# Kernel optimization log

Hardware: AMD Instinct MI355X
Metric: run time of the kernel (lower is better)

The kernel has to match this reference:

```python
import jax, jax.numpy as jnp
import numpy as np

N = 16384
M = 4096

def setup_inputs() -> dict:
    key = jax.random.key(0)
    kA, kB = jax.random.split(key)
    A = jax.random.normal(kA, (N,), dtype=jnp.float32)
    B = jax.random.normal(kB, (N, M), dtype=jnp.float32)
    return {"A": A, "B": B}

def reference(A, B):
    # C = diag(A) @ B == scale row i of B by A[i]
    return A[:, None] * B
```

## Files before the change

kernel.cpp:

```cpp
#include <hip/hip_runtime.h>


__global__ __launch_bounds__(256) void rowscale_f4_kernel(
    const float* __restrict__ A,
    const float4* __restrict__ B,
    float4* __restrict__ C,
    unsigned int nvec,
    unsigned int row_shift)
{
    unsigned int i = blockIdx.x * blockDim.x + threadIdx.x;
    unsigned int stride = gridDim.x * blockDim.x;
    for (; i < nvec; i += stride) {
        unsigned int row = i >> row_shift;
        float a = A[row];
        float4 b = B[i];
        float4 c;
        c.x = a * b.x;
        c.y = a * b.y;
        c.z = a * b.z;
        c.w = a * b.w;
        C[i] = c;
    }
}

__global__ __launch_bounds__(256) void rowscale_f4_div_kernel(
    const float* __restrict__ A,
    const float4* __restrict__ B,
    float4* __restrict__ C,
    unsigned int nvec,
    unsigned int vec_per_row)
{
    unsigned int i = blockIdx.x * blockDim.x + threadIdx.x;
    unsigned int stride = gridDim.x * blockDim.x;
    for (; i < nvec; i += stride) {
        unsigned int row = i / vec_per_row;
        float a = A[row];
        float4 b = B[i];
        float4 c;
        c.x = a * b.x;
        c.y = a * b.y;
        c.z = a * b.z;
        c.w = a * b.w;
        C[i] = c;
    }
}

extern "C" void kernel_launch(void* const* d_in, const int* in_sizes, int n_in,
                              void* d_out, int out_size, void* d_ws, size_t ws_size,
                              hipStream_t stream) {
    const float* A = (const float*)d_in[0];
    const float* B = (const float*)d_in[1];
    float* C = (float*)d_out;

    const unsigned int N = (unsigned int)in_sizes[0];
    const unsigned int total = (unsigned int)in_sizes[1];
    const unsigned int M = total / N;
    const unsigned int nvec = total / 4;
    const unsigned int vec_per_row = M / 4;

    const int block = 256;
    unsigned int blocks_needed = (nvec + block - 1) / block;
    int grid = (int)(blocks_needed < 2048u ? blocks_needed : 2048u);

    if ((vec_per_row & (vec_per_row - 1)) == 0) {
        unsigned int shift = 0;
        while ((1u << shift) < vec_per_row) ++shift;
        rowscale_f4_kernel<<<grid, block, 0, stream>>>(
            A, (const float4*)B, (float4*)C, nvec, shift);
    } else {
        rowscale_f4_div_kernel<<<grid, block, 0, stream>>>(
            A, (const float4*)B, (float4*)C, nvec, vec_per_row);
    }
}
```

Baseline: 109.9 us.

## Assign rows to blocks with unrolled nontemporal float4 loads and stores

Restructures the kernel so each block processes whole rows, loading the scale factor once per row instead of once per vector. For 4096-wide rows it issues four independent float4 loads per thread before the stores, raising memory-level parallelism, and all B reads and C writes use nontemporal hints to avoid polluting cache. The grid grows to up to 4096 blocks. The risk is that nontemporal stores or the coarser row-level scheduling could interact poorly with the memory system.

```diff
diff --git a/kernel.cpp b/kernel.cpp
--- a/kernel.cpp
+++ b/kernel.cpp
@@ -1,47 +1,37 @@
 #include <hip/hip_runtime.h>
 
 
-__global__ __launch_bounds__(256) void rowscale_f4_kernel(
+typedef float fvec4 __attribute__((ext_vector_type(4)));
+
+__global__ __launch_bounds__(256) void rowscale_rows_kernel(
     const float* __restrict__ A,
-    const float4* __restrict__ B,
-    float4* __restrict__ C,
-    unsigned int nvec,
-    unsigned int row_shift)
-{
-    unsigned int i = blockIdx.x * blockDim.x + threadIdx.x;
-    unsigned int stride = gridDim.x * blockDim.x;
-    for (; i < nvec; i += stride) {
-        unsigned int row = i >> row_shift;
-        float a = A[row];
-        float4 b = B[i];
-        float4 c;
-        c.x = a * b.x;
-        c.y = a * b.y;
-        c.z = a * b.z;
-        c.w = a * b.w;
-        C[i] = c;
-    }
-}
-
-__global__ __launch_bounds__(256) void rowscale_f4_div_kernel(
-    const float* __restrict__ A,
-    const float4* __restrict__ B,
-    float4* __restrict__ C,
-    unsigned int nvec,
+    const fvec4* __restrict__ B,
+    fvec4* __restrict__ C,
+    unsigned int nrows,
     unsigned int vec_per_row)
 {
-    unsigned int i = blockIdx.x * blockDim.x + threadIdx.x;
-    unsigned int stride = gridDim.x * blockDim.x;
-    for (; i < nvec; i += stride) {
-        unsigned int row = i / vec_per_row;
-        float a = A[row];
-        float4 b = B[i];
-        float4 c;
-        c.x = a * b.x;
-        c.y = a * b.y;
-        c.z = a * b.z;
-        c.w = a * b.w;
-        C[i] = c;
+    const unsigned int tid = threadIdx.x;
+    for (unsigned int row = blockIdx.x; row < nrows; row += gridDim.x) {
+        const float a = A[row];
+        const unsigned int base = row * vec_per_row;
+        const fvec4* brow = B + base;
+        fvec4* crow = C + base;
+
+        if (vec_per_row == 1024u) {
+            fvec4 b0 = __builtin_nontemporal_load(&brow[tid]);
+            fvec4 b1 = __builtin_nontemporal_load(&brow[tid + 256u]);
+            fvec4 b2 = __builtin_nontemporal_load(&brow[tid + 512u]);
+            fvec4 b3 = __builtin_nontemporal_load(&brow[tid + 768u]);
+            __builtin_nontemporal_store(a * b0, &crow[tid]);
+            __builtin_nontemporal_store(a * b1, &crow[tid + 256u]);
+            __builtin_nontemporal_store(a * b2, &crow[tid + 512u]);
+            __builtin_nontemporal_store(a * b3, &crow[tid + 768u]);
+        } else {
+            for (unsigned int j = tid; j < vec_per_row; j += blockDim.x) {
+                fvec4 b = __builtin_nontemporal_load(&brow[j]);
+                __builtin_nontemporal_store(a * b, &crow[j]);
+            }
+        }
     }
 }
 
@@ -49,26 +39,16 @@
                               void* d_out, int out_size, void* d_ws, size_t ws_size,
                               hipStream_t stream) {
     const float* A = (const float*)d_in[0];
-    const float* B = (const float*)d_in[1];
-    float* C = (float*)d_out;
+    const fvec4* B = (const fvec4*)d_in[1];
+    fvec4* C = (fvec4*)d_out;
 
     const unsigned int N = (unsigned int)in_sizes[0];
     const unsigned int total = (unsigned int)in_sizes[1];
     const unsigned int M = total / N;
-    const unsigned int nvec = total / 4;
     const unsigned int vec_per_row = M / 4;
 
     const int block = 256;
-    unsigned int blocks_needed = (nvec + block - 1) / block;
-    int grid = (int)(blocks_needed < 2048u ? blocks_needed : 2048u);
+    unsigned int grid = N < 4096u ? N : 4096u;
 
-    if ((vec_per_row & (vec_per_row - 1)) == 0) {
-        unsigned int shift = 0;
-        while ((1u << shift) < vec_per_row) ++shift;
-        rowscale_f4_kernel<<<grid, block, 0, stream>>>(
-            A, (const float4*)B, (float4*)C, nvec, shift);
-    } else {
-        rowscale_f4_div_kernel<<<grid, block, 0, stream>>>(
-            A, (const float4*)B, (float4*)C, nvec, vec_per_row);
-    }
+    rowscale_rows_kernel<<<grid, block, 0, stream>>>(A, B, C, N, vec_per_row);
 }
```

After: 91.91 us. 1.2x faster.
